# Optimization experiments

Measured on AMD Instinct MI355X. Metric: run time of the kernel, lower is better.

The kernel has to match this reference:

```python
import jax, jax.numpy as jnp
import numpy as np

T, B, D, H, R, S, M = 1024, 16, 512, 8, 32, 16, 16
TQ = R + T + S   # query length
KL = M + R + T   # key/value length
NEG_INF = -1e8


def setup_inputs() -> dict:
    key = jax.random.key(0)
    ks = jax.random.split(key, 12)
    utterance = jax.random.normal(ks[0], (T, B, D), jnp.float32)
    right_context = jax.random.normal(ks[1], (R, B, D), jnp.float32)
    summary = jax.random.normal(ks[2], (S, B, D), jnp.float32)
    mems = jax.random.normal(ks[3], (M, B, D), jnp.float32)
    # valid lengths in [T//2, T]; force max == T so data-dependent shapes are static
    lengths = jax.random.randint(ks[4], (B,), T // 2, T + 1).at[0].set(T).astype(jnp.int64)
    # block-streaming style mask: query i may only attend to keys <= i + M
    q_idx = jnp.arange(TQ)[:, None]
    k_idx = jnp.arange(KL)[None, :]
    attention_mask = k_idx > (q_idx + M)  # True = masked
    scale = 0.02
    Wq = jax.random.normal(ks[5], (D, D), jnp.float32) * scale
    bq = jnp.zeros((D,), jnp.float32)
    Wkv = jax.random.normal(ks[6], (2 * D, D), jnp.float32) * scale
    bkv = jnp.zeros((2 * D,), jnp.float32)
    Wo = jax.random.normal(ks[7], (D, D), jnp.float32) * scale
    bo = jnp.zeros((D,), jnp.float32)
    return dict(utterance=utterance, lengths=lengths, right_context=right_context,
                summary=summary, mems=mems, attention_mask=attention_mask,
                Wq=Wq, bq=bq, Wkv=Wkv, bkv=bkv, Wo=Wo, bo=bo)


def _split_heads(x):
    # (L, B, D) -> (B*H, L, D//H), matching torch .view(-1, B*H, d).transpose(0, 1)
    L = x.shape[0]
    return x.reshape(L, B * H, D // H).transpose(1, 0, 2)


def reference(utterance, lengths, right_context, summary, mems, attention_mask,
              Wq, bq, Wkv, bkv, Wo, bo):
    d_head = D // H
    scaling = d_head ** -0.5

    query_in = jnp.concatenate([right_context, utterance, summary], axis=0)   # (TQ, B, D)
    kv_in = jnp.concatenate([mems, right_context, utterance], axis=0)         # (KL, B, D)

    query = query_in @ Wq.T + bq
    kv = kv_in @ Wkv.T + bkv
    k, v = jnp.split(kv, 2, axis=2)

    q = _split_heads(query)  # (B*H, TQ, d)
    kh = _split_heads(k)     # (B*H, KL, d)
    vh = _split_heads(v)

    w = jnp.einsum('nqd,nkd->nqk', q * scaling, kh).astype(jnp.float32)
    w = jnp.where(attention_mask[None, :, :], NEG_INF, w)

    # padding mask (B > 1 path): klengths = lengths + M + right_context_blocks_length
    rcbl = TQ - jnp.max(lengths) - S  # == R since max(lengths) == T
    klengths = lengths + M + rcbl
    pad_mask = jnp.arange(KL)[None, :] >= klengths[:, None]  # (B, KL)
    w = w.reshape(B, H, TQ, KL)
    w = jnp.where(pad_mask[:, None, None, :], NEG_INF, w)
    w = w.reshape(B * H, TQ, KL)

    probs = jax.nn.softmax(w, axis=-1)  # dropout p=0.0
    attn = jnp.einsum('nqk,nkd->nqd', probs, vh)          # (B*H, TQ, d)
    attn = attn.transpose(1, 0, 2).reshape(TQ, B, D)

    out = attn @ Wo.T + bo                                # (TQ, B, D)
    output_right_context = out[:TQ - S]                    # (R+T, B, D)
    output_mems = jnp.clip(out[TQ - S:], -10.0, 10.0)      # tanh_on_mem=False
    return output_right_context, output_mems[:-1]          # (S-1, B, D)
```

## Files before the change

### kernel.cpp

```cpp
#include <hip/hip_runtime.h>

#define T_   1024
#define B_   16
#define D_   512
#define H_   8
#define R_   32
#define S_   16
#define M_   16
#define TQ_  1072
#define KL_  1072
#define DH_  64
#define NROW 17152
#define K_   512
#define LQ_  268
#define QSCALE 0.18033688f

typedef unsigned short u16;
using bf16x8 = __attribute__((ext_vector_type(8))) short;
using f32x4  = __attribute__((ext_vector_type(4))) float;
using u16x4  = __attribute__((ext_vector_type(4))) unsigned short;

__device__ __forceinline__ u16 f2bf(float f) {
    unsigned int u = __builtin_bit_cast(unsigned int, f);
    unsigned int r = u + 0x7fffu + ((u >> 16) & 1u);
    return (u16)(r >> 16);
}

__device__ __forceinline__ void gload_lds16(const u16* g, u16* l) {
    __builtin_amdgcn_global_load_lds(
        (const __attribute__((address_space(1))) unsigned int*)g,
        (__attribute__((address_space(3))) unsigned int*)l,
        16, 0, 0);
}

__global__ void k_convert4(const float4* __restrict__ utt, const float4* __restrict__ rc,
                           const float4* __restrict__ smr, const float4* __restrict__ mems,
                           const float4* __restrict__ Wq, const float4* __restrict__ Wkv,
                           const float4* __restrict__ Wo,
                           u16x4* __restrict__ xall,
                           u16x4* __restrict__ wq, u16x4* __restrict__ wkv,
                           u16x4* __restrict__ wo)
{
    const int N4 = 17408 * D_ / 4;
    const int MB = M_ * B_ * D_ / 4;
    const int RB = MB + R_ * B_ * D_ / 4;
    const int UB = RB + T_ * B_ * D_ / 4;
    const int W1 = D_ * D_ / 4, W2 = 2 * D_ * D_ / 4;
    for (int i = blockIdx.x * blockDim.x + threadIdx.x; i < N4;
         i += gridDim.x * blockDim.x) {
        float4 v;
        if (i < MB)      v = mems[i];
        else if (i < RB) v = rc[i - MB];
        else if (i < UB) v = utt[i - RB];
        else             v = smr[i - UB];
        xall[i] = (u16x4){f2bf(v.x), f2bf(v.y), f2bf(v.z), f2bf(v.w)};
        if (i < W1) { v = Wq[i];  wq[i]  = (u16x4){f2bf(v.x), f2bf(v.y), f2bf(v.z), f2bf(v.w)}; }
        if (i < W2) { v = Wkv[i]; wkv[i] = (u16x4){f2bf(v.x), f2bf(v.y), f2bf(v.z), f2bf(v.w)}; }
        if (i < W1) { v = Wo[i];  wo[i]  = (u16x4){f2bf(v.x), f2bf(v.y), f2bf(v.z), f2bf(v.w)}; }
    }
}

#define GEMM_CORE(A_PTR, W_PTR)                                                  \
    __shared__ __align__(16) u16 As[256 * 64];                                   \
    __shared__ __align__(16) u16 Bs[128 * 64];                                   \
    const int w    = threadIdx.x >> 6;                                           \
    const int lane = threadIdx.x & 63;                                           \
    const int col = lane & 15, quad = lane >> 4;                                 \
    const int lrow = lane >> 3;                                        \
    const int lchk = (lane & 7) ^ lrow;                      \
    const u16* gA = (A_PTR) + (size_t)(tm * 256 + w * 64 + lrow) * K_ + lchk * 8;\
    const u16* gB = (W_PTR) + (size_t)(w * 32 + lrow) * K_ + lchk * 8;           \
    f32x4 acc[4][8];                                                             \
    _Pragma("unroll")                                                            \
    for (int mi = 0; mi < 4; mi++)                                               \
        _Pragma("unroll")                                                        \
        for (int ni = 0; ni < 8; ni++) acc[mi][ni] = (f32x4){0.f,0.f,0.f,0.f};   \
    for (int k0 = 0; k0 < K_; k0 += 64) {                                        \
        __syncthreads();                                                         \
        _Pragma("unroll")                                                        \
        for (int i = 0; i < 8; i++)                                              \
            gload_lds16(gA + k0 + (size_t)i * 8 * K_,                            \
                        &As[(w * 64 + i * 8) * 64]);                             \
        _Pragma("unroll")                                                        \
        for (int j = 0; j < 4; j++)                                              \
            gload_lds16(gB + k0 + (size_t)j * 8 * K_,                            \
                        &Bs[(w * 32 + j * 8) * 64]);                             \
        __syncthreads();                                                         \
        _Pragma("unroll")                                                        \
        for (int kh = 0; kh < 2; kh++) {                                         \
            bf16x8 aF[4], bF[8];                                                 \
            _Pragma("unroll")                                                    \
            for (int mi = 0; mi < 4; mi++)                                       \
                aF[mi] = *(const bf16x8*)&As[(w * 64 + mi * 16 + col) * 64       \
                             + (((kh * 4 + quad) ^ (col & 7)) * 8)];             \
            _Pragma("unroll")                                                    \
            for (int ni = 0; ni < 8; ni++)                                       \
                bF[ni] = *(const bf16x8*)&Bs[(ni * 16 + col) * 64                \
                             + (((kh * 4 + quad) ^ (col & 7)) * 8)];             \
            _Pragma("unroll")                                                    \
            for (int mi = 0; mi < 4; mi++)                                       \
                _Pragma("unroll")                                                \
                for (int ni = 0; ni < 8; ni++)                                   \
                    acc[mi][ni] = __builtin_amdgcn_mfma_f32_16x16x32_bf16(       \
                                      aF[mi], bF[ni], acc[mi][ni], 0, 0, 0);     \
        }                                                                        \
    }

__global__ __launch_bounds__(256, 2)
void k_gemm_qkv(const u16* __restrict__ xall,
                const u16* __restrict__ wqp, const u16* __restrict__ wkvp,
                const float* __restrict__ bq, const float* __restrict__ bkv,
                u16* __restrict__ qb, u16* __restrict__ kb, u16* __restrict__ vt)
{
    const int bid = blockIdx.x;
    const int tn = (bid % 96) >> 3;
    const int tm = (bid / 96) * 8 + (bid & 7);
    if (tm >= 67) return;

    const bool isQ = tn < 4;
    const int wr0 = (isQ ? tn : tn - 4) * 128;
    const u16* Ab = isQ ? (xall + (size_t)256 * K_) : xall;
    const u16* Wb = (isQ ? wqp : wkvp) + (size_t)wr0 * K_;
    const float* bias = isQ ? bq : bkv;

    GEMM_CORE(Ab, Wb)

#pragma unroll
    for (int ni = 0; ni < 8; ni++) {
        int gcol = wr0 + ni * 16 + col;
        float bs = bias[gcol];
        if (!isQ && gcol >= 512) {
            int f  = gcol - 512;
            int lq = tm * 4 + w;
#pragma unroll
            for (int r = 0; r < 4; r++) {
                int bb = quad * 4 + r;
                u16x4 pk;
#pragma unroll
                for (int mi = 0; mi < 4; mi++)
                    pk[mi] = f2bf(acc[mi][ni][r] + bs);
                *(u16x4*)&vt[(((size_t)bb * LQ_ + lq) * 512 + f) * 4] = pk;
            }
            continue;
        }
#pragma unroll
        for (int mi = 0; mi < 4; mi++) {
#pragma unroll
            for (int r = 0; r < 4; r++) {
                int mrow = tm * 256 + w * 64 + mi * 16 + quad * 4 + r;
                float val = acc[mi][ni][r] + bs;
                if (isQ) qb[(size_t)mrow * 512 + gcol] = f2bf(val * QSCALE);
                else     kb[(size_t)mrow * 512 + gcol] = f2bf(val);
            }
        }
    }
}

__global__ __launch_bounds__(256, 2)
void k_gemm_o(const u16* __restrict__ A, const u16* __restrict__ W,
              const float* __restrict__ bias, float* __restrict__ Co)
{
    const int bid = blockIdx.x;
    const int tn = (bid % 32) >> 3;
    const int tm = (bid / 32) * 8 + (bid & 7);
    if (tm >= 67) return;

    const u16* Wb = W + (size_t)tn * 128 * K_;

    GEMM_CORE(A, Wb)

#pragma unroll
    for (int ni = 0; ni < 8; ni++) {
        int gcol = tn * 128 + ni * 16 + col;
        float bs = bias[gcol];
#pragma unroll
        for (int mi = 0; mi < 4; mi++) {
#pragma unroll
            for (int r = 0; r < 4; r++) {
                int mrow = tm * 256 + w * 64 + mi * 16 + quad * 4 + r;
                int l = mrow >> 4;
                if (l == TQ_ - 1) continue;
                float val = acc[mi][ni][r] + bs;
                if (l >= TQ_ - S_) val = fminf(10.0f, fmaxf(-10.0f, val));
                Co[(size_t)mrow * 512 + gcol] = val;
            }
        }
    }
}

__global__ __launch_bounds__(256, 2)
void k_attn5(const u16* __restrict__ qbuf, const u16* __restrict__ kb,
             const u16* __restrict__ vt, const int* __restrict__ lenp,
             u16* __restrict__ attnb)
{
    __shared__ __align__(16) u16 Ks[2][64 * 64];
    __shared__ __align__(16) u16 Vs[2][64 * 64];
    __shared__ __align__(16) u16 Ps[4][16 * 64];

    const int blk  = blockIdx.x;
    const int qblk = 16 - (blk >> 7);
    const int bh   = blk & 127;
    const int b = bh >> 3, h = bh & 7;
    const int tid = threadIdx.x;
    const int w = tid >> 6, lane = tid & 63;
    const int col = lane & 15, quad = lane >> 4;

    int stride = (lenp[1] == 0) ? 2 : 1;
    int maxlen = 0;
    for (int i = 0; i < B_; i++) maxlen = max(maxlen, lenp[i * stride]);
    const int klen = lenp[b * stride] + M_ + (TQ_ - maxlen - S_);

    const int q0 = qblk * 64;
    const int qw = q0 + w * 16;
    const int q  = qw + col;

    int qrow = min(q, TQ_ - 1);
    const u16* qp = qbuf + ((size_t)qrow * B_ + b) * D_ + h * DH_ + quad * 8;
    bf16x8 bq0 = *(const bf16x8*)(qp);
    bf16x8 bq1 = *(const bf16x8*)(qp + 32);

    const int s0 = tid, s1 = tid + 256;
    const u16* kbase = kb + (size_t)b * 512 + h * DH_;
    size_t kof0 = (size_t)(s0 >> 3) * 8192 + (size_t)(((s0 & 7) ^ ((s0 >> 3) & 7)) * 8);
    size_t kof1 = (size_t)(s1 >> 3) * 8192 + (size_t)(((s1 & 7) ^ ((s1 >> 3) & 7)) * 8);
    const u16* vbase = vt + ((size_t)b * LQ_ * 512 + (size_t)h * DH_) * 4;
    auto vchunk = [](int s) -> size_t {
        int fp = s >> 4;
        int lq = (s & 15) ^ (fp & 15);
        return (size_t)lq * 2048 + (size_t)fp * 8;
    };
    const size_t vof0 = vchunk(s0), vof1 = vchunk(s1);

    float li = 0.f;
    f32x4 o[4];
#pragma unroll
    for (int g = 0; g < 4; g++) o[g] = (f32x4){0.f, 0.f, 0.f, 0.f};

    const int nk = min(q0 + 64 + M_, klen);
    const int numkt = (nk + 63) >> 6;
    u16* pw = &Ps[w][0];

    gload_lds16(kbase + kof0, &Ks[0][(size_t)w * 512]);
    gload_lds16(kbase + kof1, &Ks[0][2048 + (size_t)w * 512]);
    gload_lds16(vbase + vof0, &Vs[0][(size_t)w * 512]);
    gload_lds16(vbase + vof1, &Vs[0][2048 + (size_t)w * 512]);

    for (int kt = 0; kt < numkt; kt++) {
        const int kn0 = kt * 64;
        const int cur = kt & 1;
        __syncthreads();
        if (kt + 1 < numkt) {
            const size_t kstep = (size_t)(kn0 + 64) * 8192;
            const size_t vstep = (size_t)(kt + 1) * 32768;
            gload_lds16(kbase + kstep + kof0, &Ks[cur ^ 1][(size_t)w * 512]);
            gload_lds16(kbase + kstep + kof1, &Ks[cur ^ 1][2048 + (size_t)w * 512]);
            gload_lds16(vbase + vstep + vof0, &Vs[cur ^ 1][(size_t)w * 512]);
            gload_lds16(vbase + vstep + vof1, &Vs[cur ^ 1][2048 + (size_t)w * 512]);
        }

        f32x4 sc[4];
#pragma unroll
        for (int g = 0; g < 4; g++) {
            int key = g * 16 + col;
            bf16x8 a0 = *(const bf16x8*)&Ks[cur][key * 64 + ((quad ^ (key & 7)) * 8)];
            bf16x8 a1 = *(const bf16x8*)&Ks[cur][key * 64 + (((4 + quad) ^ (key & 7)) * 8)];
            f32x4 z = {0.f, 0.f, 0.f, 0.f};
            z = __builtin_amdgcn_mfma_f32_16x16x32_bf16(a0, bq0, z, 0, 0, 0);
            z = __builtin_amdgcn_mfma_f32_16x16x32_bf16(a1, bq1, z, 0, 0, 0);
            sc[g] = z;
        }

        const bool needmask = (kn0 + 63 > qw + M_) || (kn0 + 63 >= klen);
        if (needmask) {
#pragma unroll
            for (int g = 0; g < 4; g++)
#pragma unroll
                for (int r = 0; r < 4; r++) {
                    int key = kn0 + g * 16 + quad * 4 + r;
                    bool valid = (key <= q + M_) && (key < klen);
                    sc[g][r] = valid ? sc[g][r] : -1e8f;
                }
        }

#pragma unroll
        for (int g = 0; g < 4; g++) {
            u16x4 pk;
#pragma unroll
            for (int r = 0; r < 4; r++) {
                float p = __builtin_amdgcn_exp2f(sc[g][r]);
                li += p;
                pk[r] = f2bf(p);
            }
            int kc = g * 2 + (quad >> 1);
            *(u16x4*)&pw[col * 64 + ((kc ^ (col & 7)) * 8) + (quad & 1) * 4] = pk;
        }

        bf16x8 ap0 = *(const bf16x8*)&pw[col * 64 + ((quad ^ (col & 7)) * 8)];
        bf16x8 ap1 = *(const bf16x8*)&pw[col * 64 + (((4 + quad) ^ (col & 7)) * 8)];
#pragma unroll
        for (int g = 0; g < 4; g++) {
            int d = g * 16 + col;
            int fp = d >> 1, fo = (d & 1) * 4;
            bf16x8 bv[2];
#pragma unroll
            for (int hh = 0; hh < 2; hh++) {
                int lqA = hh * 8 + quad * 2;
                int posA = fp * 16 + (lqA ^ (fp & 15));
                int posB = fp * 16 + ((lqA + 1) ^ (fp & 15));
                u16x4 loA = *(const u16x4*)&Vs[cur][posA * 8 + fo];
                u16x4 loB = *(const u16x4*)&Vs[cur][posB * 8 + fo];
                bf16x8 t;
                t[0] = loA[0]; t[1] = loA[1]; t[2] = loA[2]; t[3] = loA[3];
                t[4] = loB[0]; t[5] = loB[1]; t[6] = loB[2]; t[7] = loB[3];
                bv[hh] = t;
            }
            o[g] = __builtin_amdgcn_mfma_f32_16x16x32_bf16(ap0, bv[0], o[g], 0, 0, 0);
            o[g] = __builtin_amdgcn_mfma_f32_16x16x32_bf16(ap1, bv[1], o[g], 0, 0, 0);
        }
    }

    li += __shfl_xor(li, 16);
    li += __shfl_xor(li, 32);
#pragma unroll
    for (int r = 0; r < 4; r++) {
        float lr = __shfl(li, quad * 4 + r, 16);
        float inv = 1.0f / lr;
        int qo = qw + quad * 4 + r;
        if (qo < TQ_) {
#pragma unroll
            for (int g = 0; g < 4; g++) {
                int d = h * DH_ + g * 16 + col;
                attnb[((size_t)qo * B_ + b) * D_ + d] = f2bf(o[g][r] * inv);
            }
        }
    }
}

extern "C" void kernel_launch(void* const* d_in, const int* in_sizes, int n_in,
                              void* d_out, int out_size, void* d_ws, size_t ws_size,
                              hipStream_t stream)
{
    const float* utt  = (const float*)d_in[0];
    const int*   len  = (const int*)  d_in[1];
    const float* rc   = (const float*)d_in[2];
    const float* smr  = (const float*)d_in[3];
    const float* mems = (const float*)d_in[4];
    const float* Wq   = (const float*)d_in[6];
    const float* bq   = (const float*)d_in[7];
    const float* Wkv  = (const float*)d_in[8];
    const float* bkv  = (const float*)d_in[9];
    const float* Wo   = (const float*)d_in[10];
    const float* bo   = (const float*)d_in[11];

    char* ws = (char*)d_ws;
    size_t off = 0;
    auto alloc = [&](size_t bytes) -> void* {
        void* p = ws + off;
        off += (bytes + 255) & ~(size_t)255;
        return p;
    };
    u16* xall = (u16*)alloc((size_t)17408 * D_ * 2);
    u16* wq   = (u16*)alloc((size_t)D_ * D_ * 2);
    u16* wkv  = (u16*)alloc((size_t)2 * D_ * D_ * 2);
    u16* wo   = (u16*)alloc((size_t)D_ * D_ * 2);
    u16* qb   = (u16*)alloc((size_t)NROW * D_ * 2);
    u16* kb   = (u16*)alloc((size_t)NROW * D_ * 2);
    u16* vt   = (u16*)alloc((size_t)B_ * LQ_ * 512 * 4 * 2 + 65536);
    u16* attnb = xall;

    k_convert4<<<2048, 256, 0, stream>>>((const float4*)utt, (const float4*)rc,
                                         (const float4*)smr, (const float4*)mems,
                                         (const float4*)Wq, (const float4*)Wkv,
                                         (const float4*)Wo,
                                         (u16x4*)xall,
                                         (u16x4*)wq, (u16x4*)wkv, (u16x4*)wo);
    k_gemm_qkv<<<9 * 96, 256, 0, stream>>>(xall, wq, wkv, bq, bkv, qb, kb, vt);
    k_attn5<<<17 * 128, 256, 0, stream>>>(qb, kb, vt, len, attnb);
    k_gemm_o<<<9 * 32, 256, 0, stream>>>(attnb, wo, bo, (float*)d_out);
}
```

Measured before the change: 210.1 us.

## Shrink GEMM tiles to 128x128 with 2x2 warp layout and cheaper bf16 packing

The shared GEMM core moves from 256x128 tiles (each warp 64x128) to 128x128 tiles with a 2x2 warp grid. This roughly doubles block counts for the QKV and output projections and raises the launch-bounds occupancy target to 4 blocks. Float-to-bf16 conversion switches from round-to-nearest-even to plain round-half-up with a perm-based pair pack, which cuts ALU work in the convert, epilogue and softmax paths. In exchange, the smaller tiles reuse each loaded element less, and the rounding changes slightly on ties.

```diff
diff --git a/kernel.cpp b/kernel.cpp
--- a/kernel.cpp
+++ b/kernel.cpp
@@ -20,10 +20,13 @@
 using f32x4  = __attribute__((ext_vector_type(4))) float;
 using u16x4  = __attribute__((ext_vector_type(4))) unsigned short;
 
-__device__ __forceinline__ u16 f2bf(float f) {
-    unsigned int u = __builtin_bit_cast(unsigned int, f);
-    unsigned int r = u + 0x7fffu + ((u >> 16) & 1u);
-    return (u16)(r >> 16);
+__device__ __forceinline__ u16 f2bf_fast(float f) {
+    return (u16)((__builtin_bit_cast(unsigned int, f) + 0x8000u) >> 16);
+}
+__device__ __forceinline__ unsigned int packbf2(float a, float b) {
+    unsigned int ua = __builtin_bit_cast(unsigned int, a) + 0x8000u;
+    unsigned int ub = __builtin_bit_cast(unsigned int, b) + 0x8000u;
+    return __builtin_amdgcn_perm(ub, ua, 0x07060302u);
 }
 
 __device__ __forceinline__ void gload_lds16(const u16* g, u16* l) {
@@ -37,9 +40,9 @@
                            const float4* __restrict__ smr, const float4* __restrict__ mems,
                            const float4* __restrict__ Wq, const float4* __restrict__ Wkv,
                            const float4* __restrict__ Wo,
-                           u16x4* __restrict__ xall,
-                           u16x4* __restrict__ wq, u16x4* __restrict__ wkv,
-                           u16x4* __restrict__ wo)
+                           uint2* __restrict__ xall,
+                           uint2* __restrict__ wq, uint2* __restrict__ wkv,
+                           uint2* __restrict__ wo)
 {
     const int N4 = 17408 * D_ / 4;
     const int MB = M_ * B_ * D_ / 4;
@@ -53,34 +56,35 @@
         else if (i < RB) v = rc[i - MB];
         else if (i < UB) v = utt[i - RB];
         else             v = smr[i - UB];
-        xall[i] = (u16x4){f2bf(v.x), f2bf(v.y), f2bf(v.z), f2bf(v.w)};
-        if (i < W1) { v = Wq[i];  wq[i]  = (u16x4){f2bf(v.x), f2bf(v.y), f2bf(v.z), f2bf(v.w)}; }
-        if (i < W2) { v = Wkv[i]; wkv[i] = (u16x4){f2bf(v.x), f2bf(v.y), f2bf(v.z), f2bf(v.w)}; }
-        if (i < W1) { v = Wo[i];  wo[i]  = (u16x4){f2bf(v.x), f2bf(v.y), f2bf(v.z), f2bf(v.w)}; }
+        xall[i] = (uint2){packbf2(v.x, v.y), packbf2(v.z, v.w)};
+        if (i < W1) { v = Wq[i];  wq[i]  = (uint2){packbf2(v.x, v.y), packbf2(v.z, v.w)}; }
+        if (i < W2) { v = Wkv[i]; wkv[i] = (uint2){packbf2(v.x, v.y), packbf2(v.z, v.w)}; }
+        if (i < W1) { v = Wo[i];  wo[i]  = (uint2){packbf2(v.x, v.y), packbf2(v.z, v.w)}; }
     }
 }
 
 #define GEMM_CORE(A_PTR, W_PTR)                                                  \
-    __shared__ __align__(16) u16 As[256 * 64];                                   \
+    __shared__ __align__(16) u16 As[128 * 64];                                   \
     __shared__ __align__(16) u16 Bs[128 * 64];                                   \
     const int w    = threadIdx.x >> 6;                                           \
     const int lane = threadIdx.x & 63;                                           \
     const int col = lane & 15, quad = lane >> 4;                                 \
+    const int wm = w >> 1, wn = w & 1;                                           \
     const int lrow = lane >> 3;                                        \
     const int lchk = (lane & 7) ^ lrow;                      \
-    const u16* gA = (A_PTR) + (size_t)(tm * 256 + w * 64 + lrow) * K_ + lchk * 8;\
+    const u16* gA = (A_PTR) + (size_t)(tm * 128 + w * 32 + lrow) * K_ + lchk * 8;\
     const u16* gB = (W_PTR) + (size_t)(w * 32 + lrow) * K_ + lchk * 8;           \
-    f32x4 acc[4][8];                                                             \
+    f32x4 acc[4][4];                                                             \
     _Pragma("unroll")                                                            \
     for (int mi = 0; mi < 4; mi++)                                               \
         _Pragma("unroll")                                                        \
-        for (int ni = 0; ni < 8; ni++) acc[mi][ni] = (f32x4){0.f,0.f,0.f,0.f};   \
+        for (int ni = 0; ni < 4; ni++) acc[mi][ni] = (f32x4){0.f,0.f,0.f,0.f};   \
     for (int k0 = 0; k0 < K_; k0 += 64) {                                        \
         __syncthreads();                                                         \
         _Pragma("unroll")                                                        \
-        for (int i = 0; i < 8; i++)                                              \
+        for (int i = 0; i < 4; i++)                                              \
             gload_lds16(gA + k0 + (size_t)i * 8 * K_,                            \
-                        &As[(w * 64 + i * 8) * 64]);                             \
+                        &As[(w * 32 + i * 8) * 64]);                             \
         _Pragma("unroll")                                                        \
         for (int j = 0; j < 4; j++)                                              \
             gload_lds16(gB + k0 + (size_t)j * 8 * K_,                            \
@@ -88,25 +92,25 @@
         __syncthreads();                                                         \
         _Pragma("unroll")                                                        \
         for (int kh = 0; kh < 2; kh++) {                                         \
-            bf16x8 aF[4], bF[8];                                                 \
+            bf16x8 aF[4], bF[4];                                                 \
             _Pragma("unroll")                                                    \
             for (int mi = 0; mi < 4; mi++)                                       \
-                aF[mi] = *(const bf16x8*)&As[(w * 64 + mi * 16 + col) * 64       \
+                aF[mi] = *(const bf16x8*)&As[(wm * 64 + mi * 16 + col) * 64      \
                              + (((kh * 4 + quad) ^ (col & 7)) * 8)];             \
             _Pragma("unroll")                                                    \
-            for (int ni = 0; ni < 8; ni++)                                       \
-                bF[ni] = *(const bf16x8*)&Bs[(ni * 16 + col) * 64                \
+            for (int ni = 0; ni < 4; ni++)                                       \
+                bF[ni] = *(const bf16x8*)&Bs[(wn * 64 + ni * 16 + col) * 64      \
                              + (((kh * 4 + quad) ^ (col & 7)) * 8)];             \
             _Pragma("unroll")                                                    \
             for (int mi = 0; mi < 4; mi++)                                       \
                 _Pragma("unroll")                                                \
-                for (int ni = 0; ni < 8; ni++)                                   \
+                for (int ni = 0; ni < 4; ni++)                                   \
                     acc[mi][ni] = __builtin_amdgcn_mfma_f32_16x16x32_bf16(       \
                                       aF[mi], bF[ni], acc[mi][ni], 0, 0, 0);     \
         }                                                                        \
     }
 
-__global__ __launch_bounds__(256, 2)
+__global__ __launch_bounds__(256, 4)
 void k_gemm_qkv(const u16* __restrict__ xall,
                 const u16* __restrict__ wqp, const u16* __restrict__ wkvp,
                 const float* __restrict__ bq, const float* __restrict__ bkv,
@@ -115,7 +119,7 @@
     const int bid = blockIdx.x;
     const int tn = (bid % 96) >> 3;
     const int tm = (bid / 96) * 8 + (bid & 7);
-    if (tm >= 67) return;
+    if (tm >= 134) return;
 
     const bool isQ = tn < 4;
     const int wr0 = (isQ ? tn : tn - 4) * 128;
@@ -126,20 +130,18 @@
     GEMM_CORE(Ab, Wb)
 
 #pragma unroll
-    for (int ni = 0; ni < 8; ni++) {
-        int gcol = wr0 + ni * 16 + col;
+    for (int ni = 0; ni < 4; ni++) {
+        int gcol = wr0 + wn * 64 + ni * 16 + col;
         float bs = bias[gcol];
         if (!isQ && gcol >= 512) {
             int f  = gcol - 512;
-            int lq = tm * 4 + w;
+            int lq = tm * 2 + wm;
 #pragma unroll
             for (int r = 0; r < 4; r++) {
                 int bb = quad * 4 + r;
-                u16x4 pk;
-#pragma unroll
-                for (int mi = 0; mi < 4; mi++)
-                    pk[mi] = f2bf(acc[mi][ni][r] + bs);
-                *(u16x4*)&vt[(((size_t)bb * LQ_ + lq) * 512 + f) * 4] = pk;
+                uint2 pk = {packbf2(acc[0][ni][r] + bs, acc[1][ni][r] + bs),
+                            packbf2(acc[2][ni][r] + bs, acc[3][ni][r] + bs)};
+                *(uint2*)&vt[(((size_t)bb * LQ_ + lq) * 512 + f) * 4] = pk;
             }
             continue;
         }
@@ -147,37 +149,37 @@
         for (int mi = 0; mi < 4; mi++) {
 #pragma unroll
             for (int r = 0; r < 4; r++) {
-                int mrow = tm * 256 + w * 64 + mi * 16 + quad * 4 + r;
+                int mrow = tm * 128 + wm * 64 + mi * 16 + quad * 4 + r;
                 float val = acc[mi][ni][r] + bs;
-                if (isQ) qb[(size_t)mrow * 512 + gcol] = f2bf(val * QSCALE);
-                else     kb[(size_t)mrow * 512 + gcol] = f2bf(val);
-            }
-        }
-    }
-}
-
-__global__ __launch_bounds__(256, 2)
+                if (isQ) qb[(size_t)mrow * 512 + gcol] = f2bf_fast(val * QSCALE);
+                else     kb[(size_t)mrow * 512 + gcol] = f2bf_fast(val);
+            }
+        }
+    }
+}
+
+__global__ __launch_bounds__(256, 4)
 void k_gemm_o(const u16* __restrict__ A, const u16* __restrict__ W,
               const float* __restrict__ bias, float* __restrict__ Co)
 {
     const int bid = blockIdx.x;
     const int tn = (bid % 32) >> 3;
     const int tm = (bid / 32) * 8 + (bid & 7);
-    if (tm >= 67) return;
+    if (tm >= 134) return;
 
     const u16* Wb = W + (size_t)tn * 128 * K_;
 
     GEMM_CORE(A, Wb)
 
 #pragma unroll
-    for (int ni = 0; ni < 8; ni++) {
-        int gcol = tn * 128 + ni * 16 + col;
+    for (int ni = 0; ni < 4; ni++) {
+        int gcol = tn * 128 + wn * 64 + ni * 16 + col;
         float bs = bias[gcol];
 #pragma unroll
         for (int mi = 0; mi < 4; mi++) {
 #pragma unroll
             for (int r = 0; r < 4; r++) {
-                int mrow = tm * 256 + w * 64 + mi * 16 + quad * 4 + r;
+                int mrow = tm * 128 + wm * 64 + mi * 16 + quad * 4 + r;
                 int l = mrow >> 4;
                 if (l == TQ_ - 1) continue;
                 float val = acc[mi][ni][r] + bs;
@@ -189,7 +191,7 @@
 }
 
 __global__ __launch_bounds__(256, 2)
-void k_attn5(const u16* __restrict__ qbuf, const u16* __restrict__ kb,
+void k_attn6(const u16* __restrict__ qbuf, const u16* __restrict__ kb,
              const u16* __restrict__ vt, const int* __restrict__ lenp,
              u16* __restrict__ attnb)
 {
@@ -284,15 +286,14 @@
 
 #pragma unroll
         for (int g = 0; g < 4; g++) {
-            u16x4 pk;
-#pragma unroll
-            for (int r = 0; r < 4; r++) {
-                float p = __builtin_amdgcn_exp2f(sc[g][r]);
-                li += p;
-                pk[r] = f2bf(p);
-            }
+            float p0 = __builtin_amdgcn_exp2f(sc[g][0]);
+            float p1 = __builtin_amdgcn_exp2f(sc[g][1]);
+            float p2 = __builtin_amdgcn_exp2f(sc[g][2]);
+            float p3 = __builtin_amdgcn_exp2f(sc[g][3]);
+            li += (p0 + p1) + (p2 + p3);
+            uint2 pk = {packbf2(p0, p1), packbf2(p2, p3)};
             int kc = g * 2 + (quad >> 1);
-            *(u16x4*)&pw[col * 64 + ((kc ^ (col & 7)) * 8) + (quad & 1) * 4] = pk;
+            *(uint2*)&pw[col * 64 + ((kc ^ (col & 7)) * 8) + (quad & 1) * 4] = pk;
         }
 
         bf16x8 ap0 = *(const bf16x8*)&pw[col * 64 + ((quad ^ (col & 7)) * 8)];
@@ -330,7 +331,7 @@
 #pragma unroll
             for (int g = 0; g < 4; g++) {
                 int d = h * DH_ + g * 16 + col;
-                attnb[((size_t)qo * B_ + b) * D_ + d] = f2bf(o[g][r] * inv);
+                attnb[((size_t)qo * B_ + b) * D_ + d] = f2bf_fast(o[g][r] * inv);
             }
         }
     }
@@ -372,9 +373,9 @@
                                          (const float4*)smr, (const float4*)mems,
                                          (const float4*)Wq, (const float4*)Wkv,
                                          (const float4*)Wo,
-                                         (u16x4*)xall,
-                                         (u16x4*)wq, (u16x4*)wkv, (u16x4*)wo);
-    k_gemm_qkv<<<9 * 96, 256, 0, stream>>>(xall, wq, wkv, bq, bkv, qb, kb, vt);
-    k_attn5<<<17 * 128, 256, 0, stream>>>(qb, kb, vt, len, attnb);
-    k_gemm_o<<<9 * 32, 256, 0, stream>>>(attnb, wo, bo, (float*)d_out);
-}
+                                         (uint2*)xall,
+                                         (uint2*)wq, (uint2*)wkv, (uint2*)wo);
+    k_gemm_qkv<<<17 * 96, 256, 0, stream>>>(xall, wq, wkv, bq, bkv, qb, kb, vt);
+    k_attn6<<<17 * 128, 256, 0, stream>>>(qb, kb, vt, len, attnb);
+    k_gemm_o<<<17 * 32, 256, 0, stream>>>(attnb, wo, bo, (float*)d_out);
+}
```

Result: slower. 219.7 us (+4.6%).
